# Performance work log

Hardware: AMD Instinct MI355X
Metric: run time of the kernel (lower is better)

The kernel has to match this reference:

```python
import jax, jax.numpy as jnp
import numpy as np

D_MODEL = 1024
N_HEADS = 16
D_K = D_MODEL // N_HEADS


def setup_inputs() -> dict:
    key = jax.random.key(0)
    ks = jax.random.split(key, 9)
    s = 0.02
    return {
        "x": jax.random.normal(ks[0], (4, 2048, D_MODEL), dtype=jnp.float32),
        "WQ_w": jax.random.normal(ks[1], (D_MODEL, D_MODEL), dtype=jnp.float32) * s,
        "WQ_b": jax.random.normal(ks[2], (D_MODEL,), dtype=jnp.float32) * s,
        "WK_w": jax.random.normal(ks[3], (D_MODEL, D_MODEL), dtype=jnp.float32) * s,
        "WK_b": jax.random.normal(ks[4], (D_MODEL,), dtype=jnp.float32) * s,
        "WV_w": jax.random.normal(ks[5], (D_MODEL, D_MODEL), dtype=jnp.float32) * s,
        "WV_b": jax.random.normal(ks[6], (D_MODEL,), dtype=jnp.float32) * s,
        "Wo_w": jax.random.normal(ks[7], (D_MODEL, D_MODEL), dtype=jnp.float32) * s,
        "Wo_b": jax.random.normal(ks[8], (D_MODEL,), dtype=jnp.float32) * s,
    }


def _rope_cache(T, dtype):
    half = D_K // 2
    freq = 1.0 / (10000.0 ** (2.0 * jnp.arange(half, dtype=dtype) / D_K))
    angles = jnp.arange(T, dtype=dtype)[:, None] * freq[None, :]  # [T, half]
    return jnp.cos(angles), jnp.sin(angles)


def _apply_rope(x, cos, sin):
    # x: [B, H, T, d_k]; cos/sin: [T, d_k//2] broadcast over B,H
    half = x.shape[-1] // 2
    x1, x2 = x[..., :half], x[..., half:]
    return jnp.concatenate([x1 * cos - x2 * sin, x1 * sin + x2 * cos], axis=-1)


def reference(x, WQ_w, WQ_b, WK_w, WK_b, WV_w, WV_b, Wo_w, Wo_b):
    B, T, D = x.shape

    def proj(w, b):
        y = jnp.einsum('btd,ed->bte', x, w) + b
        return y.reshape(B, T, N_HEADS, D_K).transpose(0, 2, 1, 3)  # [B,H,T,d_k]

    q = proj(WQ_w, WQ_b)
    k = proj(WK_w, WK_b)
    v = proj(WV_w, WV_b)

    cos, sin = _rope_cache(T, x.dtype)
    q = _apply_rope(q, cos, sin)
    k = _apply_rope(k, cos, sin)

    scores = jnp.einsum('bhqd,bhkd->bhqk', q, k) / jnp.sqrt(jnp.asarray(D_K, x.dtype))
    causal = jnp.tril(jnp.ones((T, T), dtype=bool))
    scores = jnp.where(causal[None, None, :, :], scores, -jnp.inf)
    attn = jax.nn.softmax(scores, axis=-1)
    out = jnp.einsum('bhqk,bhkd->bhqd', attn, v)
    out = out.transpose(0, 2, 1, 3).reshape(B, T, D)
    return jnp.einsum('btd,ed->bte', out, Wo_w) + Wo_b
```

## Files before the change

### kernel.cpp

```cpp
#include <hip/hip_runtime.h>
#include <math.h>

#define DM 1024
#define NH 16
#define DK 64
#define BB 4
#define TT 2048
#define MTOT (BB*TT)

typedef __bf16 bf16x8 __attribute__((ext_vector_type(8)));
typedef short  s16x4  __attribute__((ext_vector_type(4)));
typedef float  f32x4  __attribute__((ext_vector_type(4)));

__device__ __forceinline__ short f2bf_s(float f) {
    __bf16 h = (__bf16)f;
    return __builtin_bit_cast(short, h);
}

__device__ __forceinline__ float exp2_fast(float x) {
    float r;
    asm("v_exp_f32 %0, %1" : "=v"(r) : "v"(x));
    return r;
}

__device__ __forceinline__ void async_copy16(unsigned short* lds, const unsigned short* g) {
    __builtin_amdgcn_global_load_lds(
        (const __attribute__((address_space(1))) unsigned int*)g,
        (__attribute__((address_space(3))) unsigned int*)lds, 16, 0, 0);
}

__global__ __launch_bounds__(256)
void cvt_all_kernel(const float* __restrict__ x,
                    const float* __restrict__ wq, const float* __restrict__ wk,
                    const float* __restrict__ wv, const float* __restrict__ wo,
                    unsigned short* __restrict__ xb,
                    unsigned short* __restrict__ wqb, unsigned short* __restrict__ wkb,
                    unsigned short* __restrict__ wvb, unsigned short* __restrict__ wob)
{
    const int XB = (MTOT * DM) / 1024;
    int bz = blockIdx.x;
    const float* src; unsigned short* dst; int blk;
    if (bz < XB) { src = x; dst = xb; blk = bz; }
    else {
        int t = bz - XB, which = t >> 10;
        blk = t & 1023;
        if (which == 0)      { src = wq; dst = wqb; }
        else if (which == 1) { src = wk; dst = wkb; }
        else if (which == 2) { src = wv; dst = wvb; }
        else                 { src = wo; dst = wob; }
    }
    int i = blk * 256 + threadIdx.x;
    float4 v = ((const float4*)src)[i];
    ushort4 o;
    o.x = (unsigned short)f2bf_s(v.x); o.y = (unsigned short)f2bf_s(v.y);
    o.z = (unsigned short)f2bf_s(v.z); o.w = (unsigned short)f2bf_s(v.w);
    ((ushort4*)dst)[i] = o;
}

template<int MODE>
__global__ __launch_bounds__(256, 3)
void gemm_bf16_kernel(const unsigned short* __restrict__ X,
                      const unsigned short* __restrict__ W0, const float* __restrict__ b0,
                      const unsigned short* __restrict__ W1, const float* __restrict__ b1,
                      const unsigned short* __restrict__ W2, const float* __restrict__ b2,
                      void* __restrict__ Y0, void* __restrict__ Y1, void* __restrict__ Y2)
{
    const unsigned short* W; const float* bias; void* Yv;
    const int z = blockIdx.z;
    if (z == 0)      { W = W0; bias = b0; Yv = Y0; }
    else if (z == 1) { W = W1; bias = b1; Yv = Y1; }
    else             { W = W2; bias = b2; Yv = Y2; }

    __shared__ __align__(16) unsigned short As[128 * 64];
    __shared__ __align__(16) unsigned short Bs[128 * 64];

    const int tid  = threadIdx.x;
    const int w    = tid >> 6, lane = tid & 63;
    const int quad = lane >> 4, lq = lane & 15;
    const int bm = blockIdx.x * 128, bn = blockIdx.y * 128;
    const int wm = (w >> 1) * 64,   wn = (w & 1) * 64;

    const int srow = lane >> 3;
    const int sg   = (lane & 7) ^ srow;
    const int soff = sg * 8;

    f32x4 acc[4][4];
    #pragma unroll
    for (int i = 0; i < 4; ++i)
        #pragma unroll
        for (int j = 0; j < 4; ++j)
            acc[i][j] = {0.f, 0.f, 0.f, 0.f};

    for (int k0 = 0; k0 < DM; k0 += 64) {
        #pragma unroll
        for (int c = 0; c < 4; ++c) {
            int r0 = w * 32 + c * 8;
            async_copy16(&As[r0 * 64], &X[(size_t)(bm + r0 + srow) * DM + k0 + soff]);
            async_copy16(&Bs[r0 * 64], &W[(size_t)(bn + r0 + srow) * DM + k0 + soff]);
        }
        __syncthreads();

        #pragma unroll
        for (int ks = 0; ks < 2; ++ks) {
            const int gsw = ((ks << 2) + quad) ^ (lq & 7);
            bf16x8 af[4], bfr[4];
            #pragma unroll
            for (int i = 0; i < 4; ++i)
                af[i] = *(const bf16x8*)&As[(wm + i*16 + lq) * 64 + gsw * 8];
            #pragma unroll
            for (int j = 0; j < 4; ++j)
                bfr[j] = *(const bf16x8*)&Bs[(wn + j*16 + lq) * 64 + gsw * 8];
            #pragma unroll
            for (int i = 0; i < 4; ++i)
                #pragma unroll
                for (int j = 0; j < 4; ++j)
                    acc[i][j] = __builtin_amdgcn_mfma_f32_16x16x32_bf16(af[i], bfr[j], acc[i][j], 0, 0, 0);
        }
        __syncthreads();
    }

    if (MODE == 0) {
        #pragma unroll
        for (int j = 0; j < 4; ++j) {
            int n = bn + wn + j*16 + lq;
            float bv = bias[n];
            #pragma unroll
            for (int i = 0; i < 4; ++i)
                #pragma unroll
                for (int r = 0; r < 4; ++r) {
                    int m = bm + wm + i*16 + quad*4 + r;
                    ((float*)Yv)[(size_t)m * DM + n] = acc[i][j][r] + bv;
                }
        }
    } else if (z == 2) {
        #pragma unroll
        for (int j = 0; j < 4; ++j) {
            int n = bn + wn + j*16 + lq;
            float bv = bias[n];
            int h = n >> 6, dk = n & 63;
            #pragma unroll
            for (int i = 0; i < 4; ++i) {
                int m0 = bm + wm + i*16 + quad*4;
                int b = m0 >> 11, t0 = m0 & 2047;
                ushort4 o;
                o.x = (unsigned short)f2bf_s(acc[i][j][0] + bv);
                o.y = (unsigned short)f2bf_s(acc[i][j][1] + bv);
                o.z = (unsigned short)f2bf_s(acc[i][j][2] + bv);
                o.w = (unsigned short)f2bf_s(acc[i][j][3] + bv);
                *(ushort4*)&((unsigned short*)Yv)[((size_t)(b * NH + h) * DK + dk) * TT + t0] = o;
            }
        }
    } else {
        const float QSC = (z == 0) ? 0.125f * 1.44269504f : 1.0f;
        const int h = (bn + wn) >> 6;
        const int b = (bm + wm) >> 11;
        const int tb0 = ((bm + wm) & 2047) + quad * 4;
        #pragma unroll
        for (int jp = 0; jp < 2; ++jp) {
            int dk1 = jp * 16 + lq;
            float freq = exp2f(-(float)dk1 * 0.4152410118f);
            float bv1 = bias[bn + wn + dk1];
            float bv2 = bias[bn + wn + dk1 + 32];
            float s1, c1, s16v, c16v, sb, cb;
            __sincosf(freq, &s1, &c1);
            __sincosf(16.0f * freq, &s16v, &c16v);
            __sincosf((float)tb0 * freq, &sb, &cb);
            #pragma unroll
            for (int i = 0; i < 4; ++i) {
                float cr = cb, sr = sb;
                #pragma unroll
                for (int r = 0; r < 4; ++r) {
                    int t = tb0 + i*16 + r;
                    float v1 = acc[i][jp][r]     + bv1;
                    float v2 = acc[i][jp + 2][r] + bv2;
                    float o1 = (v1 * cr - v2 * sr) * QSC;
                    float o2 = (v1 * sr + v2 * cr) * QSC;
                    size_t base = ((size_t)(b * NH + h) * TT + t) << 6;
                    unsigned int pk = (unsigned int)(unsigned short)f2bf_s(o1)
                                    | ((unsigned int)(unsigned short)f2bf_s(o2) << 16);
                    *(unsigned int*)&((unsigned short*)Yv)[base + 2*dk1] = pk;
                    float cn = cr * c1 - sr * s1;
                    sr = cr * s1 + sr * c1;
                    cr = cn;
                }
                float cbn = cb * c16v - sb * s16v;
                sb = cb * s16v + sb * c16v;
                cb = cbn;
            }
        }
    }
}

__global__ __launch_bounds__(256, 4)
void attn_kernel(const unsigned short* __restrict__ Q, const unsigned short* __restrict__ K,
                 const unsigned short* __restrict__ Vt_g, unsigned short* __restrict__ ctx)
{
    __shared__ __align__(16) unsigned short KV[2][2][64 * 64];

    const int tid  = threadIdx.x;
    const int w    = tid >> 6, lane = tid & 63;
    const int quad = lane >> 4, lq = lane & 15;
    const int bh = blockIdx.x;
    const int qt = 31 - blockIdx.y;
    const size_t kbase = (size_t)bh * TT * DK;
    const size_t vbase = (size_t)bh * DK * TT;

    const int srow = lane >> 3;
    const int sg   = (lane & 7) ^ srow;
    const unsigned short* Ksrc = &K[kbase + (size_t)(w*16 + srow) * DK + sg*8];
    const unsigned short* Vsrc = &Vt_g[vbase + (size_t)(w*16 + srow) * TT + sg*8];

    auto issue = [&](int kb, int buf) {
        unsigned short* Kd = &KV[buf][0][w*16*64];
        unsigned short* Vd = &KV[buf][1][w*16*64];
        const unsigned short* ks0 = Ksrc + (size_t)kb * 64 * DK;
        const unsigned short* vs0 = Vsrc + (size_t)kb * 64;
        async_copy16(Kd,          ks0);
        async_copy16(Kd + 8*64,   ks0 + 8*DK);
        async_copy16(Vd,          vs0);
        async_copy16(Vd + 8*64,   vs0 + (size_t)8*TT);
    };

    const int qrow = qt*64 + w*16 + lq;
    bf16x8 qf[2];
    qf[0] = *(const bf16x8*)&Q[kbase + (size_t)qrow * DK + quad*8];
    qf[1] = *(const bf16x8*)&Q[kbase + (size_t)qrow * DK + 32 + quad*8];

    f32x4 accO[4];
    float l_i = 0.f;
    #pragma unroll
    for (int dt = 0; dt < 4; ++dt) accO[dt] = {0.f,0.f,0.f,0.f};

    issue(0, 0);
    for (int kb = 0; kb <= qt; ++kb) {
        __syncthreads();
        if (kb < qt) issue(kb + 1, (kb + 1) & 1);

        const unsigned short* Kb_ = &KV[kb & 1][0][0];
        const unsigned short* Vb_ = &KV[kb & 1][1][0];

        f32x4 st[4];
        #pragma unroll
        for (int nt = 0; nt < 4; ++nt) st[nt] = {0.f,0.f,0.f,0.f};
        #pragma unroll
        for (int ks = 0; ks < 2; ++ks) {
            bf16x8 kfh[4];
            #pragma unroll
            for (int nt = 0; nt < 4; ++nt)
                kfh[nt] = *(const bf16x8*)&Kb_[(nt*16 + lq) * 64 +
                                (((ks << 2) + quad) ^ (lq & 7)) * 8];
            __builtin_amdgcn_s_setprio(1);
            #pragma unroll
            for (int nt = 0; nt < 4; ++nt)
                st[nt] = __builtin_amdgcn_mfma_f32_16x16x32_bf16(kfh[nt], qf[ks], st[nt], 0, 0, 0);
            __builtin_amdgcn_s_setprio(0);
        }
        if (kb == qt) {
            #pragma unroll
            for (int nt = 0; nt < 4; ++nt)
                #pragma unroll
                for (int r = 0; r < 4; ++r) {
                    int kc = kb*64 + nt*16 + quad*4 + r;
                    if (kc > qrow) st[nt][r] = -1e30f;
                }
        }
        s16x4 p[4];
        #pragma unroll
        for (int nt = 0; nt < 4; ++nt)
            #pragma unroll
            for (int r = 0; r < 4; ++r) {
                float e = exp2_fast(st[nt][r]);
                l_i += e;
                p[nt][r] = f2bf_s(e);
            }

        #pragma unroll
        for (int ktp = 0; ktp < 2; ++ktp) {
            s16x4 vbh[2][4];
            #pragma unroll
            for (int k2 = 0; k2 < 2; ++k2) {
                int kt = ktp*2 + k2;
                #pragma unroll
                for (int dt = 0; dt < 4; ++dt)
                    vbh[k2][dt] = *(const s16x4*)&Vb_[(dt*16 + lq) * 64 +
                                    (((kt << 1) + (quad >> 1)) ^ (lq & 7)) * 8 +
                                    (quad & 1) * 4];
            }
            __builtin_amdgcn_s_setprio(1);
            #pragma unroll
            for (int k2 = 0; k2 < 2; ++k2)
                #pragma unroll
                for (int dt = 0; dt < 4; ++dt)
                    accO[dt] = __builtin_amdgcn_mfma_f32_16x16x16bf16_1k(
                        p[ktp*2 + k2], vbh[k2][dt], accO[dt], 0, 0, 0);
            __builtin_amdgcn_s_setprio(0);
        }
    }

    const int b = bh >> 4, h = bh & 15;
    float l = l_i;
    l += __shfl_xor(l, 16, 64);
    l += __shfl_xor(l, 32, 64);
    float linv = 1.0f / l;
    f32x4 il4;
    #pragma unroll
    for (int r = 0; r < 4; ++r) il4[r] = __shfl(linv, quad*4 + r, 64);
    #pragma unroll
    for (int r = 0; r < 4; ++r) {
        int t = qt*64 + w*16 + quad*4 + r;
        size_t ob = ((size_t)b * TT + t) * DM + h * DK;
        #pragma unroll
        for (int dt = 0; dt < 4; ++dt)
            ((__bf16*)ctx)[ob + dt*16 + lq] = (__bf16)(accO[dt][r] * il4[r]);
    }
}

extern "C" void kernel_launch(void* const* d_in, const int* in_sizes, int n_in,
                              void* d_out, int out_size, void* d_ws, size_t ws_size,
                              hipStream_t stream)
{
    const float* x   = (const float*)d_in[0];
    const float* WQw = (const float*)d_in[1];
    const float* WQb = (const float*)d_in[2];
    const float* WKw = (const float*)d_in[3];
    const float* WKb = (const float*)d_in[4];
    const float* WVw = (const float*)d_in[5];
    const float* WVb = (const float*)d_in[6];
    const float* WOw = (const float*)d_in[7];
    const float* WOb = (const float*)d_in[8];
    float* out = (float*)d_out;

    unsigned short* ws  = (unsigned short*)d_ws;
    unsigned short* xb  = ws;
    unsigned short* wqb = xb  + (size_t)MTOT * DM;
    unsigned short* wkb = wqb + (size_t)DM * DM;
    unsigned short* wvb = wkb + (size_t)DM * DM;
    unsigned short* wob = wvb + (size_t)DM * DM;
    unsigned short* Qb  = wob + (size_t)DM * DM;
    unsigned short* Kb  = Qb  + (size_t)MTOT * DM;
    unsigned short* Vb  = Kb  + (size_t)MTOT * DM;
    unsigned short* Vtb = Vb  + (size_t)MTOT * DM;
    unsigned short* ctxb = Vb;

    cvt_all_kernel<<<(MTOT*DM)/1024 + 4*(DM*DM)/1024, 256, 0, stream>>>(
        x, WQw, WKw, WVw, WOw, xb, wqb, wkb, wvb, wob);

    gemm_bf16_kernel<1><<<dim3(MTOT/128, DM/128, 3), 256, 0, stream>>>(
        xb, wqb, WQb, wkb, WKb, wvb, WVb, Qb, Kb, Vtb);

    attn_kernel<<<dim3(BB*NH, 32), 256, 0, stream>>>(Qb, Kb, Vtb, ctxb);

    gemm_bf16_kernel<0><<<dim3(MTOT/128, DM/128, 1), 256, 0, stream>>>(
        ctxb, wob, WOb, wob, WOb, wob, WOb, out, out, out);
}
```

Before: 240.2 us.

## Permute V^T layout for 128-bit LDS reads and compute row sums via MFMA

The V projection epilogue now writes V^T with a permuted time index inside each 64-key block, so the attention kernel can fetch V fragments with one 8-element LDS read per head-dim tile instead of two 4-element reads. The softmax denominator is no longer accumulated with scalar adds and cross-lane shuffles; it comes from an extra MFMA of P against a ones vector, which also places the sums directly in the output row layout. This trades a few extra MFMAs per block for fewer VALU adds and LDS instructions, and the row sums now use the bf16-rounded probabilities, matching the values used for P·V.

```diff
diff --git a/kernel.cpp b/kernel.cpp
--- a/kernel.cpp
+++ b/kernel.cpp
@@ -10,6 +10,7 @@
 
 typedef __bf16 bf16x8 __attribute__((ext_vector_type(8)));
 typedef short  s16x4  __attribute__((ext_vector_type(4)));
+typedef short  s16x8  __attribute__((ext_vector_type(8)));
 typedef float  f32x4  __attribute__((ext_vector_type(4)));
 
 __device__ __forceinline__ short f2bf_s(float f) {
@@ -142,12 +143,15 @@
             for (int i = 0; i < 4; ++i) {
                 int m0 = bm + wm + i*16 + quad*4;
                 int b = m0 >> 11, t0 = m0 & 2047;
+                int u0 = t0 & 63;
+                int t0n = (t0 & ~63) | (((u0 >> 5) & 1) << 5)
+                        | (((u0 >> 2) & 3) << 3) | (((u0 >> 4) & 1) << 2);
                 ushort4 o;
                 o.x = (unsigned short)f2bf_s(acc[i][j][0] + bv);
                 o.y = (unsigned short)f2bf_s(acc[i][j][1] + bv);
                 o.z = (unsigned short)f2bf_s(acc[i][j][2] + bv);
                 o.w = (unsigned short)f2bf_s(acc[i][j][3] + bv);
-                *(ushort4*)&((unsigned short*)Yv)[((size_t)(b * NH + h) * DK + dk) * TT + t0] = o;
+                *(ushort4*)&((unsigned short*)Yv)[((size_t)(b * NH + h) * DK + dk) * TT + t0n] = o;
             }
         }
     } else {
@@ -226,8 +230,9 @@
     qf[0] = *(const bf16x8*)&Q[kbase + (size_t)qrow * DK + quad*8];
     qf[1] = *(const bf16x8*)&Q[kbase + (size_t)qrow * DK + 32 + quad*8];
 
+    const s16x4 ones = {(short)0x3F80, (short)0x3F80, (short)0x3F80, (short)0x3F80};
     f32x4 accO[4];
-    float l_i = 0.f;
+    f32x4 accL = {0.f, 0.f, 0.f, 0.f};
     #pragma unroll
     for (int dt = 0; dt < 4; ++dt) accO[dt] = {0.f,0.f,0.f,0.f};
 
@@ -268,43 +273,38 @@
         #pragma unroll
         for (int nt = 0; nt < 4; ++nt)
             #pragma unroll
-            for (int r = 0; r < 4; ++r) {
-                float e = exp2_fast(st[nt][r]);
-                l_i += e;
-                p[nt][r] = f2bf_s(e);
+            for (int r = 0; r < 4; ++r)
+                p[nt][r] = f2bf_s(exp2_fast(st[nt][r]));
+
+        #pragma unroll
+        for (int P = 0; P < 2; ++P) {
+            s16x8 vf[4];
+            #pragma unroll
+            for (int dt = 0; dt < 4; ++dt)
+                vf[dt] = *(const s16x8*)&Vb_[(dt*16 + lq) * 64 +
+                                (((P << 2) + quad) ^ (lq & 7)) * 8];
+            __builtin_amdgcn_s_setprio(1);
+            #pragma unroll
+            for (int k2 = 0; k2 < 2; ++k2) {
+                const int kt = P*2 + k2;
+                accL = __builtin_amdgcn_mfma_f32_16x16x16bf16_1k(p[kt], ones, accL, 0, 0, 0);
+                #pragma unroll
+                for (int dt = 0; dt < 4; ++dt) {
+                    s16x4 vs;
+                    if (k2) vs = __builtin_shufflevector(vf[dt], vf[dt], 4, 5, 6, 7);
+                    else    vs = __builtin_shufflevector(vf[dt], vf[dt], 0, 1, 2, 3);
+                    accO[dt] = __builtin_amdgcn_mfma_f32_16x16x16bf16_1k(
+                        p[kt], vs, accO[dt], 0, 0, 0);
+                }
             }
-
-        #pragma unroll
-        for (int ktp = 0; ktp < 2; ++ktp) {
-            s16x4 vbh[2][4];
-            #pragma unroll
-            for (int k2 = 0; k2 < 2; ++k2) {
-                int kt = ktp*2 + k2;
-                #pragma unroll
-                for (int dt = 0; dt < 4; ++dt)
-                    vbh[k2][dt] = *(const s16x4*)&Vb_[(dt*16 + lq) * 64 +
-                                    (((kt << 1) + (quad >> 1)) ^ (lq & 7)) * 8 +
-                                    (quad & 1) * 4];
-            }
-            __builtin_amdgcn_s_setprio(1);
-            #pragma unroll
-            for (int k2 = 0; k2 < 2; ++k2)
-                #pragma unroll
-                for (int dt = 0; dt < 4; ++dt)
-                    accO[dt] = __builtin_amdgcn_mfma_f32_16x16x16bf16_1k(
-                        p[ktp*2 + k2], vbh[k2][dt], accO[dt], 0, 0, 0);
             __builtin_amdgcn_s_setprio(0);
         }
     }
 
     const int b = bh >> 4, h = bh & 15;
-    float l = l_i;
-    l += __shfl_xor(l, 16, 64);
-    l += __shfl_xor(l, 32, 64);
-    float linv = 1.0f / l;
     f32x4 il4;
     #pragma unroll
-    for (int r = 0; r < 4; ++r) il4[r] = __shfl(linv, quad*4 + r, 64);
+    for (int r = 0; r < 4; ++r) il4[r] = 1.0f / accL[r];
     #pragma unroll
     for (int r = 0; r < 4; ++r) {
         int t = qt*64 + w*16 + quad*4 + r;
```

After: 226.9 us (median of 2 runs). -5.5%, faster.
